# Performance work log

Hardware: AMD Instinct MI355X
Metric: run time of the kernel (lower is better)

The kernel has to match this reference:

```python
import jax, jax.numpy as jnp
import numpy as np

# dims: B=batch, CIN/COUT=channels, T=timesteps, K=kernel length (= T+1, since
# max_timesteps=2048 is even and CKConv bumps it to odd), DK=SIREN hidden width
B, CIN, COUT, T, DK = 32, 32, 32, 2048, 32
K = T + 1


def setup_inputs() -> dict:
    key = jax.random.key(0)
    ks = jax.random.split(key, 9)
    u = lambda k, shape, lim: jax.random.uniform(k, shape, minval=-lim, maxval=lim)
    # SIREN layer 1 (Conv1d 1->DK, k=1): first layer init uniform(-1, 1)
    w1 = u(ks[0], (DK, 1), 1.0)
    b1 = u(ks[1], (DK,), 1.0)          # torch bias init: U(-1/sqrt(fan_in)), fan_in=1
    # SIREN layer 2 (DK->DK): uniform(-sqrt(6/DK)/omega0, +), omega0=1
    siren_val = float(np.sqrt(6.0 / DK))
    w2 = u(ks[2], (DK, DK), siren_val)
    b2 = u(ks[3], (DK,), float(1.0 / np.sqrt(DK)))
    # output layer (DK -> CIN*COUT)
    w3 = u(ks[4], (CIN * COUT, DK), siren_val)
    b3 = u(ks[5], (CIN * COUT,), float(1.0 / np.sqrt(DK)))
    omega1 = jnp.asarray(1.0, jnp.float32)
    omega2 = jnp.asarray(1.0, jnp.float32)
    bias = jax.random.normal(ks[6], (COUT,), jnp.float32)   # CKConv output bias
    x = jax.random.normal(ks[7], (B, CIN, T), jnp.float32)
    rel_pos = jnp.linspace(-1.0, 1.0, K, dtype=jnp.float32)  # buffer _rel_positions
    return dict(x=x, rel_pos=rel_pos, w1=w1, b1=b1, omega1=omega1,
                w2=w2, b2=b2, omega2=omega2, w3=w3, b3=b3, bias=bias)


def reference(x, rel_pos, w1, b1, omega1, w2, b2, omega2, w3, b3, bias):
    # --- SIREN kernel network: 1x1 convs over the K positions == matmuls ---
    pos = rel_pos[None, :]                                   # (1, K)
    h = jnp.sin(omega1 * (w1 @ pos + b1[:, None]))           # (DK, K)
    h = jnp.sin(omega2 * (w2 @ h + b2[:, None]))             # (DK, K)
    kern = (w3 @ h + b3[:, None]).reshape(COUT, CIN, K)      # (COUT, CIN, K)
    # --- causal conv: left-pad by K-1 zeros, then valid cross-correlation ---
    out = jax.lax.conv_general_dilated(
        x, kern, window_strides=(1,), padding=[(K - 1, 0)],
        dimension_numbers=("NCH", "OIH", "NCH"))             # (B, COUT, T)
    return out + bias[None, :, None]
```

## Files before the change

kernel.cpp:

```cpp
#include <hip/hip_runtime.h>
#include <hip/hip_bf16.h>
#include <stdint.h>

typedef short bf16x8 __attribute__((ext_vector_type(8)));
typedef float f32x16 __attribute__((ext_vector_type(16)));

#define T 2048
#define KLEN 2049
#define DK 32
#define NCO 32
#define NCI 32
#define NB 32

#define GR 2216
#define SREF 2055
#define WT_CH 257
#define WT_ELEMS (NCI*WT_CH*NCO*8)
#define XR_ELEMS (NB*NCI*GR)

#define WT_OFF 0
#define XR_OFF (WT_ELEMS*2)
#define XRS_OFF (XR_OFF + XR_ELEMS*2)

#define CIB 528
#define GPC 1056
#define GPCP 1088
#define CPYB 17472
#define BUFB (2*CPYB)
#define LDS_TOT (2*BUFB)

__global__ __launch_bounds__(256) void gen_w(
    const float* __restrict__ rel_pos,
    const float* __restrict__ w1, const float* __restrict__ b1, const float* __restrict__ om1,
    const float* __restrict__ w2, const float* __restrict__ b2, const float* __restrict__ om2,
    const float* __restrict__ w3, const float* __restrict__ b3,
    uint16_t* __restrict__ Wt)
{
    int d = blockIdx.x;
    int tid = threadIdx.x;
    if (d >= KLEN) {
        for (int r = 0; r < 4; ++r) {
            int coci = tid + 256*r;
            int co = coci >> 5, ci = coci & 31;
            Wt[(((ci*WT_CH + (d>>3))*NCO + co)<<3) + (d&7)] = 0;
        }
        return;
    }
    int kk = 2048 - d;
    float pos = rel_pos[kk];
    __shared__ float h1[DK];
    __shared__ float h2[DK];
    if (tid < DK) h1[tid] = sinf(om1[0]*(w1[tid]*pos + b1[tid]));
    __syncthreads();
    if (tid < DK) {
        float a = b2[tid];
        for (int j = 0; j < DK; ++j) a += w2[tid*DK+j]*h1[j];
        h2[tid] = sinf(om2[0]*a);
    }
    __syncthreads();
    for (int r = 0; r < 4; ++r) {
        int coci = tid + 256*r;
        float a = b3[coci];
        for (int j = 0; j < DK; ++j) a += w3[coci*DK+j]*h2[j];
        int co = coci >> 5, ci = coci & 31;
        __hip_bfloat16 hv = __float2bfloat16(a);
        Wt[(((ci*WT_CH + (d>>3))*NCO + co)<<3) + (d&7)] = *(uint16_t*)&hv;
    }
}

__global__ __launch_bounds__(256) void gen_x(const float* __restrict__ x,
                                             uint16_t* __restrict__ xr,
                                             uint16_t* __restrict__ xrs)
{
    int idx = blockIdx.x*256 + threadIdx.x;
    if (idx >= NB*NCI*GR) return;
    int row = idx / GR;
    int g = idx - row*GR;
    int s = SREF - g;
    float v  = (s  >= 0 && s  < T) ? x[row*T + s]  : 0.f;
    int s2 = s - 1;
    float v2 = (s2 >= 0 && s2 < T) ? x[row*T + s2] : 0.f;
    __hip_bfloat16 hv = __float2bfloat16(v);
    __hip_bfloat16 hv2 = __float2bfloat16(v2);
    xr[idx]  = *(uint16_t*)&hv;
    xrs[idx] = *(uint16_t*)&hv2;
}

__device__ __forceinline__ void gld16(const uint16_t* g, char* l)
{
    typedef const __attribute__((address_space(1))) uint32_t GU;
    typedef __attribute__((address_space(3))) uint32_t LU;
    __builtin_amdgcn_global_load_lds((GU*)g, (LU*)l, 16, 0, 0);
}

__global__ __launch_bounds__(512, 4) void conv(
    const uint16_t* __restrict__ Wt, const uint16_t* __restrict__ xr,
    const float* __restrict__ bias, float* __restrict__ out)
{
    __shared__ uint4 lds4[LDS_TOT/16];
    char* ldsb = (char*)lds4;
    float* red = (float*)lds4;
    int tid = threadIdx.x;
    int b = blockIdx.x & 31;
    int q = blockIdx.x >> 5;
    int p = q & 7;
    int th = (q < 8) ? (63 - (p << 2)) : ((p << 2) + 3);
    int nw = (th + 1) >> 2;
    int g0base = 2016 - (th << 5);
    int w = tid >> 6, lane = tid & 63, n = lane & 31, hi = lane >> 5;
    int cig = w;

    int srcE[5], dstC[5];
    #pragma unroll
    for (int k = 0; k < 5; ++k) {
        int gi = tid + (k << 9);
        if (gi < 2176) {
            int cpy = gi >= GPCP;
            int j = gi - cpy*GPCP;
            dstC[k] = cpy*CPYB + (j << 4);
            if (j < GPC) {
                int ci = (j*1986) >> 16;
                int qq = j - ci*33;
                srcE[k] = (cpy ? XR_ELEMS : 0) + (b*NCI + ci)*GR + (qq << 3);
            } else srcE[k] = 0;
        } else { srcE[k] = 0; dstC[k] = -1; }
    }

    int obase = 39 - n + (hi << 3);
    int par = obase & 1;
    int bbb = cig*CIB + par*CPYB + ((obase - par) << 1);

    f32x16 acc0, acc1, acc2, acc3;
    #pragma unroll
    for (int r = 0; r < 16; ++r) { acc0[r]=0.f; acc1[r]=0.f; acc2[r]=0.f; acc3[r]=0.f; }

    #define STAGE(BUF, GOFF) { \
        _Pragma("unroll") \
        for (int k = 0; k < 5; ++k) \
            if (dstC[k] >= 0) gld16(xr + srcE[k] + (GOFF), (BUF) + dstC[k]); }

    STAGE(ldsb, g0base)
    __syncthreads();

    for (int wi = 0; wi < nw; ++wi) {
        int cur = wi & 1;
        if (wi + 1 < nw) {
            char* bufn = ldsb + (cur ^ 1)*BUFB;
            int g0n = g0base + ((wi + 1) << 7);
            STAGE(bufn, g0n)
        }
        int dcw = wi << 4;
        const char* rbase = ldsb + cur*BUFB + bbb;

        #pragma unroll
        for (int cii = 0; cii < 4; ++cii) {
            int ci = (cii << 3) + cig;
            const uint16_t* aB = Wt + (((ci*WT_CH + dcw + hi)*NCO + n) << 3);
            bf16x8 av0 = *(const bf16x8*)(aB);
            bf16x8 av1 = *(const bf16x8*)(aB + 512);
            bf16x8 av2 = *(const bf16x8*)(aB + 1024);
            bf16x8 av3 = *(const bf16x8*)(aB + 1536);
            bf16x8 av4 = *(const bf16x8*)(aB + 2048);
            bf16x8 av5 = *(const bf16x8*)(aB + 2560);
            bf16x8 av6 = *(const bf16x8*)(aB + 3072);
            bf16x8 av7 = *(const bf16x8*)(aB + 3584);
            const char* pbase = rbase + cii*(8*CIB);

            #define RDBB(MM) union { uint32_t u_[4]; bf16x8 v; } bb; { \
                const char* pp = pbase + ((MM) << 5); \
                bb.u_[0] = *(const uint32_t*)(pp); \
                bb.u_[1] = *(const uint32_t*)(pp + 4); \
                bb.u_[2] = *(const uint32_t*)(pp + 8); \
                bb.u_[3] = *(const uint32_t*)(pp + 12); }
            #define MF(AC, AV) AC = __builtin_amdgcn_mfma_f32_32x32x16_bf16(AV, bb.v, AC, 0,0,0);

            { RDBB(0)  MF(acc0, av0) }
            { RDBB(1)  MF(acc0, av1) }
            { RDBB(2)  MF(acc0, av2) MF(acc1, av0) }
            { RDBB(3)  MF(acc0, av3) MF(acc1, av1) }
            { RDBB(4)  MF(acc0, av4) MF(acc1, av2) MF(acc2, av0) }
            { RDBB(5)  MF(acc0, av5) MF(acc1, av3) MF(acc2, av1) }
            { RDBB(6)  MF(acc0, av6) MF(acc1, av4) MF(acc2, av2) MF(acc3, av0) }
            { RDBB(7)  MF(acc0, av7) MF(acc1, av5) MF(acc2, av3) MF(acc3, av1) }
            { RDBB(8)  MF(acc1, av6) MF(acc2, av4) MF(acc3, av2) }
            { RDBB(9)  MF(acc1, av7) MF(acc2, av5) MF(acc3, av3) }
            { RDBB(10) MF(acc2, av6) MF(acc3, av4) }
            { RDBB(11) MF(acc2, av7) MF(acc3, av5) }
            { RDBB(12) MF(acc3, av6) }
            { RDBB(13) MF(acc3, av7) }
            #undef MF
            #undef RDBB
        }
        __syncthreads();
    }
    #undef STAGE

    #pragma unroll
    for (int dlt = 0; dlt < 4; ++dlt) {
        f32x16 a = (dlt == 0) ? acc0 : (dlt == 1) ? acc1 : (dlt == 2) ? acc2 : acc3;
        __syncthreads();
        if (w < 4) {
            #pragma unroll
            for (int r = 0; r < 16; ++r)
                red[(w*16 + r)*64 + lane] = a[r];
        }
        __syncthreads();
        if (w >= 4) {
            #pragma unroll
            for (int r = 0; r < 16; ++r)
                red[((w-4)*16 + r)*64 + lane] += a[r];
        }
        __syncthreads();
        int t0 = (th - dlt) << 5;
        #pragma unroll
        for (int h = 0; h < 2; ++h) {
            int e = tid + (h << 9);
            int lane_e = e & 63;
            int reg = e >> 6;
            float s = 0.f;
            #pragma unroll
            for (int ww = 0; ww < 4; ++ww) s += red[(ww*16 + reg)*64 + lane_e];
            int co = (reg & 3) + ((reg >> 2) << 3) + ((lane_e >> 5) << 2);
            int t = t0 + (lane_e & 31);
            out[(b*NCO + co)*T + t] = s + bias[co];
        }
    }
}

extern "C" void kernel_launch(void* const* d_in, const int* in_sizes, int n_in,
                              void* d_out, int out_size, void* d_ws, size_t ws_size,
                              hipStream_t stream)
{
    const float* x       = (const float*)d_in[0];
    const float* rel_pos = (const float*)d_in[1];
    const float* w1  = (const float*)d_in[2];
    const float* b1  = (const float*)d_in[3];
    const float* om1 = (const float*)d_in[4];
    const float* w2  = (const float*)d_in[5];
    const float* b2  = (const float*)d_in[6];
    const float* om2 = (const float*)d_in[7];
    const float* w3  = (const float*)d_in[8];
    const float* b3  = (const float*)d_in[9];
    const float* bias = (const float*)d_in[10];
    float* out = (float*)d_out;
    char* ws = (char*)d_ws;
    uint16_t* Wt  = (uint16_t*)(ws + WT_OFF);
    uint16_t* xrp = (uint16_t*)(ws + XR_OFF);
    uint16_t* xrs = (uint16_t*)(ws + XRS_OFF);

    hipLaunchKernelGGL(gen_w, dim3(WT_CH*8), dim3(256), 0, stream,
                       rel_pos, w1, b1, om1, w2, b2, om2, w3, b3, Wt);
    int n2 = NB*NCI*GR;
    hipLaunchKernelGGL(gen_x, dim3((n2+255)/256), dim3(256), 0, stream, x, xrp, xrs);
    hipLaunchKernelGGL(conv, dim3(NB*16), dim3(512), 0, stream, Wt, xrp, bias, out);
}
```

Before: 167.4 us.

## Split triangular causal-conv work evenly across blocks with atomic output accumulation

Replaces the paired-tile assignment (16 slots per batch, each summing two output tiles' full reduction windows) with a stream-K style split: the 136 window-units per batch are divided evenly across 32 slots, so a block may handle partial reductions for several output tiles. Partial sums are combined with atomicAdd into an output buffer that a new init_out kernel prefills with the bias. This is meant to balance load and double the grid size for better CU occupancy. In exchange it adds a kernel launch, a full output write pass, atomic traffic, extra pipeline restarts and reductions at tile boundaries, and nondeterministic float summation order.

```diff
diff --git a/kernel.cpp b/kernel.cpp
--- a/kernel.cpp
+++ b/kernel.cpp
@@ -86,6 +86,13 @@
     xrs[idx] = *(uint16_t*)&hv2;
 }
 
+__global__ __launch_bounds__(256) void init_out(const float* __restrict__ bias,
+                                                float* __restrict__ out)
+{
+    int i = blockIdx.x*256 + threadIdx.x;
+    out[i] = bias[(i >> 11) & 31];
+}
+
 __device__ __forceinline__ void gld16(const uint16_t* g, char* l)
 {
     typedef const __attribute__((address_space(1))) uint32_t GU;
@@ -95,18 +102,16 @@
 
 __global__ __launch_bounds__(512, 4) void conv(
     const uint16_t* __restrict__ Wt, const uint16_t* __restrict__ xr,
-    const float* __restrict__ bias, float* __restrict__ out)
+    float* __restrict__ out)
 {
     __shared__ uint4 lds4[LDS_TOT/16];
     char* ldsb = (char*)lds4;
     float* red = (float*)lds4;
     int tid = threadIdx.x;
     int b = blockIdx.x & 31;
-    int q = blockIdx.x >> 5;
-    int p = q & 7;
-    int th = (q < 8) ? (63 - (p << 2)) : ((p << 2) + 3);
-    int nw = (th + 1) >> 2;
-    int g0base = 2016 - (th << 5);
+    int slot = blockIdx.x >> 5;
+    int U0 = (slot*17) >> 2;
+    int U1 = ((slot+1)*17) >> 2;
     int w = tid >> 6, lane = tid & 63, n = lane & 31, hi = lane >> 5;
     int cig = w;
 
@@ -130,101 +135,116 @@
     int par = obase & 1;
     int bbb = cig*CIB + par*CPYB + ((obase - par) << 1);
 
-    f32x16 acc0, acc1, acc2, acc3;
-    #pragma unroll
-    for (int r = 0; r < 16; ++r) { acc0[r]=0.f; acc1[r]=0.f; acc2[r]=0.f; acc3[r]=0.f; }
-
     #define STAGE(BUF, GOFF) { \
         _Pragma("unroll") \
         for (int k = 0; k < 5; ++k) \
             if (dstC[k] >= 0) gld16(xr + srcE[k] + (GOFF), (BUF) + dstC[k]); }
 
-    STAGE(ldsb, g0base)
-    __syncthreads();
-
-    for (int wi = 0; wi < nw; ++wi) {
-        int cur = wi & 1;
-        if (wi + 1 < nw) {
-            char* bufn = ldsb + (cur ^ 1)*BUFB;
-            int g0n = g0base + ((wi + 1) << 7);
-            STAGE(bufn, g0n)
+    int cum = 0;
+    for (int c = 0; c < 16; ++c) {
+        int nwc = (c < 8) ? (16 - c) : (c - 7);
+        int lo = (U0 > cum) ? U0 : cum;
+        int hiU = (U1 < cum + nwc) ? U1 : (cum + nwc);
+        if (lo < hiU) {
+            int th = (c < 8) ? (63 - (c << 2)) : ((c << 2) - 29);
+            int w0 = lo - cum, w1e = hiU - cum;
+            int g0base = 2016 - (th << 5);
+
+            f32x16 acc0, acc1, acc2, acc3;
+            #pragma unroll
+            for (int r = 0; r < 16; ++r) { acc0[r]=0.f; acc1[r]=0.f; acc2[r]=0.f; acc3[r]=0.f; }
+
+            __syncthreads();
+            STAGE(ldsb, g0base + (w0 << 7))
+            __syncthreads();
+
+            int cur = 0;
+            for (int wi = w0; wi < w1e; ++wi) {
+                if (wi + 1 < w1e) {
+                    char* bufn = ldsb + (cur ^ 1)*BUFB;
+                    STAGE(bufn, g0base + ((wi + 1) << 7))
+                }
+                int dcw = wi << 4;
+                const char* rbase = ldsb + cur*BUFB + bbb;
+
+                #pragma unroll
+                for (int cii = 0; cii < 4; ++cii) {
+                    int ci = (cii << 3) + cig;
+                    const uint16_t* aB = Wt + (((ci*WT_CH + dcw + hi)*NCO + n) << 3);
+                    bf16x8 av0 = *(const bf16x8*)(aB);
+                    bf16x8 av1 = *(const bf16x8*)(aB + 512);
+                    bf16x8 av2 = *(const bf16x8*)(aB + 1024);
+                    bf16x8 av3 = *(const bf16x8*)(aB + 1536);
+                    bf16x8 av4 = *(const bf16x8*)(aB + 2048);
+                    bf16x8 av5 = *(const bf16x8*)(aB + 2560);
+                    bf16x8 av6 = *(const bf16x8*)(aB + 3072);
+                    bf16x8 av7 = *(const bf16x8*)(aB + 3584);
+                    const char* pbase = rbase + cii*(8*CIB);
+
+                    #define RDBB(MM) union { uint32_t u_[4]; bf16x8 v; } bb; { \
+                        const char* pp = pbase + ((MM) << 5); \
+                        bb.u_[0] = *(const uint32_t*)(pp); \
+                        bb.u_[1] = *(const uint32_t*)(pp + 4); \
+                        bb.u_[2] = *(const uint32_t*)(pp + 8); \
+                        bb.u_[3] = *(const uint32_t*)(pp + 12); }
+                    #define MF(AC, AV) AC = __builtin_amdgcn_mfma_f32_32x32x16_bf16(AV, bb.v, AC, 0,0,0);
+
+                    { RDBB(0)  MF(acc0, av0) }
+                    { RDBB(1)  MF(acc0, av1) }
+                    { RDBB(2)  MF(acc0, av2) MF(acc1, av0) }
+                    { RDBB(3)  MF(acc0, av3) MF(acc1, av1) }
+                    { RDBB(4)  MF(acc0, av4) MF(acc1, av2) MF(acc2, av0) }
+                    { RDBB(5)  MF(acc0, av5) MF(acc1, av3) MF(acc2, av1) }
+                    { RDBB(6)  MF(acc0, av6) MF(acc1, av4) MF(acc2, av2) MF(acc3, av0) }
+                    { RDBB(7)  MF(acc0, av7) MF(acc1, av5) MF(acc2, av3) MF(acc3, av1) }
+                    { RDBB(8)  MF(acc1, av6) MF(acc2, av4) MF(acc3, av2) }
+                    { RDBB(9)  MF(acc1, av7) MF(acc2, av5) MF(acc3, av3) }
+                    { RDBB(10) MF(acc2, av6) MF(acc3, av4) }
+                    { RDBB(11) MF(acc2, av7) MF(acc3, av5) }
+                    { RDBB(12) MF(acc3, av6) }
+                    { RDBB(13) MF(acc3, av7) }
+                    #undef MF
+                    #undef RDBB
+                }
+                __syncthreads();
+                cur ^= 1;
+            }
+
+            #pragma unroll
+            for (int dlt = 0; dlt < 4; ++dlt) {
+                f32x16 a = (dlt == 0) ? acc0 : (dlt == 1) ? acc1 : (dlt == 2) ? acc2 : acc3;
+                __syncthreads();
+                if (w < 4) {
+                    #pragma unroll
+                    for (int r = 0; r < 16; ++r)
+                        red[(w*16 + r)*64 + lane] = a[r];
+                }
+                __syncthreads();
+                if (w >= 4) {
+                    #pragma unroll
+                    for (int r = 0; r < 16; ++r)
+                        red[((w-4)*16 + r)*64 + lane] += a[r];
+                }
+                __syncthreads();
+                int t0 = (th - dlt) << 5;
+                #pragma unroll
+                for (int h = 0; h < 2; ++h) {
+                    int e = tid + (h << 9);
+                    int lane_e = e & 63;
+                    int reg = e >> 6;
+                    float s = 0.f;
+                    #pragma unroll
+                    for (int ww = 0; ww < 4; ++ww) s += red[(ww*16 + reg)*64 + lane_e];
+                    int co = (reg & 3) + ((reg >> 2) << 3) + ((lane_e >> 5) << 2);
+                    int t = t0 + (lane_e & 31);
+                    atomicAdd(&out[(b*NCO + co)*T + t], s);
+                }
+            }
         }
-        int dcw = wi << 4;
-        const char* rbase = ldsb + cur*BUFB + bbb;
-
-        #pragma unroll
-        for (int cii = 0; cii < 4; ++cii) {
-            int ci = (cii << 3) + cig;
-            const uint16_t* aB = Wt + (((ci*WT_CH + dcw + hi)*NCO + n) << 3);
-            bf16x8 av0 = *(const bf16x8*)(aB);
-            bf16x8 av1 = *(const bf16x8*)(aB + 512);
-            bf16x8 av2 = *(const bf16x8*)(aB + 1024);
-            bf16x8 av3 = *(const bf16x8*)(aB + 1536);
-            bf16x8 av4 = *(const bf16x8*)(aB + 2048);
-            bf16x8 av5 = *(const bf16x8*)(aB + 2560);
-            bf16x8 av6 = *(const bf16x8*)(aB + 3072);
-            bf16x8 av7 = *(const bf16x8*)(aB + 3584);
-            const char* pbase = rbase + cii*(8*CIB);
-
-            #define RDBB(MM) union { uint32_t u_[4]; bf16x8 v; } bb; { \
-                const char* pp = pbase + ((MM) << 5); \
-                bb.u_[0] = *(const uint32_t*)(pp); \
-                bb.u_[1] = *(const uint32_t*)(pp + 4); \
-                bb.u_[2] = *(const uint32_t*)(pp + 8); \
-                bb.u_[3] = *(const uint32_t*)(pp + 12); }
-            #define MF(AC, AV) AC = __builtin_amdgcn_mfma_f32_32x32x16_bf16(AV, bb.v, AC, 0,0,0);
-
-            { RDBB(0)  MF(acc0, av0) }
-            { RDBB(1)  MF(acc0, av1) }
-            { RDBB(2)  MF(acc0, av2) MF(acc1, av0) }
-            { RDBB(3)  MF(acc0, av3) MF(acc1, av1) }
-            { RDBB(4)  MF(acc0, av4) MF(acc1, av2) MF(acc2, av0) }
-            { RDBB(5)  MF(acc0, av5) MF(acc1, av3) MF(acc2, av1) }
-            { RDBB(6)  MF(acc0, av6) MF(acc1, av4) MF(acc2, av2) MF(acc3, av0) }
-            { RDBB(7)  MF(acc0, av7) MF(acc1, av5) MF(acc2, av3) MF(acc3, av1) }
-            { RDBB(8)  MF(acc1, av6) MF(acc2, av4) MF(acc3, av2) }
-            { RDBB(9)  MF(acc1, av7) MF(acc2, av5) MF(acc3, av3) }
-            { RDBB(10) MF(acc2, av6) MF(acc3, av4) }
-            { RDBB(11) MF(acc2, av7) MF(acc3, av5) }
-            { RDBB(12) MF(acc3, av6) }
-            { RDBB(13) MF(acc3, av7) }
-            #undef MF
-            #undef RDBB
-        }
-        __syncthreads();
+        cum += nwc;
+        if (cum >= U1) break;
     }
     #undef STAGE
-
-    #pragma unroll
-    for (int dlt = 0; dlt < 4; ++dlt) {
-        f32x16 a = (dlt == 0) ? acc0 : (dlt == 1) ? acc1 : (dlt == 2) ? acc2 : acc3;
-        __syncthreads();
-        if (w < 4) {
-            #pragma unroll
-            for (int r = 0; r < 16; ++r)
-                red[(w*16 + r)*64 + lane] = a[r];
-        }
-        __syncthreads();
-        if (w >= 4) {
-            #pragma unroll
-            for (int r = 0; r < 16; ++r)
-                red[((w-4)*16 + r)*64 + lane] += a[r];
-        }
-        __syncthreads();
-        int t0 = (th - dlt) << 5;
-        #pragma unroll
-        for (int h = 0; h < 2; ++h) {
-            int e = tid + (h << 9);
-            int lane_e = e & 63;
-            int reg = e >> 6;
-            float s = 0.f;
-            #pragma unroll
-            for (int ww = 0; ww < 4; ++ww) s += red[(ww*16 + reg)*64 + lane_e];
-            int co = (reg & 3) + ((reg >> 2) << 3) + ((lane_e >> 5) << 2);
-            int t = t0 + (lane_e & 31);
-            out[(b*NCO + co)*T + t] = s + bias[co];
-        }
-    }
 }
 
 extern "C" void kernel_launch(void* const* d_in, const int* in_sizes, int n_in,
@@ -252,5 +272,6 @@
                        rel_pos, w1, b1, om1, w2, b2, om2, w3, b3, Wt);
     int n2 = NB*NCI*GR;
     hipLaunchKernelGGL(gen_x, dim3((n2+255)/256), dim3(256), 0, stream, x, xrp, xrs);
-    hipLaunchKernelGGL(conv, dim3(NB*16), dim3(512), 0, stream, Wt, xrp, bias, out);
-}
+    hipLaunchKernelGGL(init_out, dim3(NB*NCO*T/256), dim3(256), 0, stream, bias, out);
+    hipLaunchKernelGGL(conv, dim3(NB*32), dim3(512), 0, stream, Wt, xrp, out);
+}
```

Result: slower. 207.9 us (+24.2%).
